# Kernel optimization log

Measured on AMD Instinct MI355X. Metric: run time of the kernel, lower is better.

Reference implementation:

```python
import jax, jax.numpy as jnp
import numpy as np

D_MODEL = 1024
N_HEADS = 16
D_HEAD = D_MODEL // N_HEADS


def setup_inputs() -> dict:
    key = jax.random.key(0)
    k1, k2, k3 = jax.random.split(key, 3)
    x = jax.random.normal(k1, (4, 2048, D_MODEL), dtype=jnp.float32)
    # torch Linear(d, 3d, bias=False): y = x @ W.T with W [3d, d].
    # We store the transposed form W_qkv [d, 3d] so y = x @ W_qkv (same math).
    scale = 1.0 / np.sqrt(D_MODEL)
    W_qkv = jax.random.normal(k2, (D_MODEL, 3 * D_MODEL), dtype=jnp.float32) * scale
    W_o = jax.random.normal(k3, (D_MODEL, D_MODEL), dtype=jnp.float32) * scale
    return {"x": x, "W_qkv": W_qkv, "W_o": W_o}


def reference(x, W_qkv, W_o):
    B, T, C = x.shape
    qkv = x @ W_qkv                              # [B, T, 3C]
    Q, K, V = jnp.split(qkv, 3, axis=-1)
    def to_heads(t):
        return t.reshape(B, T, N_HEADS, D_HEAD).transpose(0, 2, 1, 3)  # [B,H,T,d]
    Q, K, V = to_heads(Q), to_heads(K), to_heads(V)
    scores = jnp.einsum("bhqd,bhkd->bhqk", Q, K) / np.sqrt(D_HEAD)
    attn = jax.nn.softmax(scores, axis=-1)
    # dropout is identity in eval/deterministic mode
    context = jnp.einsum("bhqk,bhkd->bhqd", attn, V)
    context = context.transpose(0, 2, 1, 3).reshape(B, T, C)
    return context @ W_o
```

## Files before the change

kernel.cpp:

```cpp
#include <hip/hip_runtime.h>
#include <hip/hip_bf16.h>

typedef __attribute__((ext_vector_type(8))) short short8;
typedef __attribute__((ext_vector_type(4))) float f32x4;
typedef __attribute__((ext_vector_type(16))) float f32x16;
typedef __attribute__((ext_vector_type(2))) unsigned int uint2v;
typedef __attribute__((ext_vector_type(4))) unsigned int uint4v;

#define SEQ    2048
#define DM     1024
#define NH     16
#define DH     64
#define NBATCH 4
#define MTOK   (NBATCH * SEQ)
#define SEG    ((size_t)NBATCH * NH * SEQ * DH)
#define QSCALE 0.18033688f

static __device__ __forceinline__ unsigned bfbits(float f) {
  unsigned u = __float_as_uint(f);
  return u + 0x7fffu + ((u >> 16) & 1u);
}
static __device__ __forceinline__ unsigned short f2bf(float f) {
  return (unsigned short)(bfbits(f) >> 16);
}
static __device__ __forceinline__ unsigned pack2bf(float lo, float hi) {
  return __builtin_amdgcn_perm(bfbits(hi), bfbits(lo), 0x07060302u);
}
static __device__ __forceinline__ unsigned pack2tr(unsigned ulo, unsigned uhi) {
  return __builtin_amdgcn_perm(uhi, ulo, 0x07060302u);
}

typedef const __attribute__((address_space(1))) unsigned int* gp_t;
typedef __attribute__((address_space(3))) unsigned int* lp_t;
static __device__ __forceinline__ void gload_lds16(const void* g, void* l) {
  __builtin_amdgcn_global_load_lds((gp_t)g, (lp_t)l, 16, 0, 0);
}

__global__ __launch_bounds__(256) void xcast(const float* __restrict__ x,
                                             unsigned short* __restrict__ xb) {
  size_t i = ((size_t)blockIdx.x * 256 + threadIdx.x) * 8;
  f32x4 a = *(const f32x4*)&x[i];
  f32x4 b = *(const f32x4*)&x[i + 4];
  uint4v s;
  s[0] = pack2bf(a[0], a[1]);
  s[1] = pack2bf(a[2], a[3]);
  s[2] = pack2bf(b[0], b[1]);
  s[3] = pack2bf(b[2], b[3]);
  *(uint4v*)&xb[i] = s;
}

__global__ __launch_bounds__(256) void transpose_w(
    const float* __restrict__ W, unsigned short* __restrict__ WT, int K, int N) {
  __shared__ float T[64][65];
  const int tid = threadIdx.x;
  const int n0 = blockIdx.x * 64;
  const int k0 = blockIdx.y * 64;
#pragma unroll
  for (int it = 0; it < 4; it++) {
    int row = it * 16 + (tid >> 4);
    int c4 = (tid & 15) * 4;
    f32x4 v = *(const f32x4*)&W[(size_t)(k0 + row) * N + n0 + c4];
#pragma unroll
    for (int j = 0; j < 4; j++) T[row][c4 + j] = v[j];
  }
  __syncthreads();
#pragma unroll
  for (int it = 0; it < 2; it++) {
    int chunk = tid + it * 256;
    int n = chunk >> 3;
    int c8 = (chunk & 7) * 8;
    uint4v s;
#pragma unroll
    for (int j = 0; j < 4; j++)
      s[j] = pack2bf(T[c8 + 2 * j][n], T[c8 + 2 * j + 1][n]);
    *(uint4v*)&WT[(size_t)(n0 + n) * K + k0 + c8] = s;
  }
}

template <int MODE>
__global__ __launch_bounds__(256) void gemm_kernel(
    const void* __restrict__ Av, const unsigned short* __restrict__ BT,
    unsigned short* __restrict__ out0, unsigned short* __restrict__ out1,
    unsigned short* __restrict__ out2, float* __restrict__ outf,
    int M, int N, int K) {
  __shared__ unsigned short As[128][64];
  __shared__ unsigned short Bs[128][64];

  const int tid = threadIdx.x;
  const int wave = tid >> 6;
  const int lane = tid & 63;
  const int quad = lane >> 4;
  const int lc = lane & 15;
  const int wr = wave >> 1;
  const int wc = wave & 1;
  const int m0 = blockIdx.y * 128;
  const int n0 = blockIdx.x * 128;
  const int xsw = lc & 7;
  const int lr8 = lane >> 3;
  const int sgo = ((lane & 7) ^ (lr8 & 7)) * 8;

  f32x4 acc[4][4];
#pragma unroll
  for (int i = 0; i < 4; i++)
#pragma unroll
    for (int j = 0; j < 4; j++) acc[i][j] = (f32x4){0.f, 0.f, 0.f, 0.f};

  for (int k0 = 0; k0 < K; k0 += 64) {
    if (MODE == 0) {
      const float* A = (const float*)Av;
#pragma unroll
      for (int i = 0; i < 4; i++) {
        int chunk = tid + i * 256;
        int r = chunk >> 3;
        int g = chunk & 7;
        int scol = (g ^ (r & 7)) * 8;
        f32x4 v0 = *(const f32x4*)&A[(size_t)(m0 + r) * K + k0 + scol];
        f32x4 v1 = *(const f32x4*)&A[(size_t)(m0 + r) * K + k0 + scol + 4];
        uint4v s;
        s[0] = pack2bf(v0[0], v0[1]);
        s[1] = pack2bf(v0[2], v0[3]);
        s[2] = pack2bf(v1[0], v1[1]);
        s[3] = pack2bf(v1[2], v1[3]);
        *(uint4v*)&As[r][g * 8] = s;
      }
    } else {
      const unsigned short* A = (const unsigned short*)Av;
#pragma unroll
      for (int it = 0; it < 4; it++) {
        int rbase = wave * 32 + it * 8;
        gload_lds16(&A[(size_t)(m0 + rbase + lr8) * K + k0 + sgo],
                    &As[rbase][0]);
      }
    }
#pragma unroll
    for (int it = 0; it < 4; it++) {
      int rbase = wave * 32 + it * 8;
      gload_lds16(&BT[(size_t)(n0 + rbase + lr8) * K + k0 + sgo],
                  &Bs[rbase][0]);
    }
    __syncthreads();

#pragma unroll
    for (int kc = 0; kc < 2; kc++) {
      short8 aA[4], bB[4];
#pragma unroll
      for (int mt = 0; mt < 4; mt++)
        aA[mt] = *(const short8*)&As[wr * 64 + mt * 16 + lc]
                                    [((kc * 4 + quad) ^ xsw) * 8];
#pragma unroll
      for (int nt = 0; nt < 4; nt++)
        bB[nt] = *(const short8*)&Bs[wc * 64 + nt * 16 + lc]
                                    [((kc * 4 + quad) ^ xsw) * 8];
#pragma unroll
      for (int mt = 0; mt < 4; mt++)
#pragma unroll
        for (int nt = 0; nt < 4; nt++)
          acc[mt][nt] = __builtin_amdgcn_mfma_f32_16x16x32_bf16(
              aA[mt], bB[nt], acc[mt][nt], 0, 0, 0);
    }
    __syncthreads();
  }

  const int c = n0 >> 10;
#pragma unroll
  for (int mt = 0; mt < 4; mt++)
#pragma unroll
    for (int nt = 0; nt < 4; nt++) {
      int rb = m0 + wr * 64 + mt * 16 + quad * 4;
      int col = n0 + wc * 64 + nt * 16 + lc;
      if (MODE == 1) {
#pragma unroll
        for (int r = 0; r < 4; r++)
          outf[(size_t)(rb + r) * N + col] = acc[mt][nt][r];
      } else {
        int rem = col & 1023;
        int h = rem >> 6;
        int dd = rem & 63;
        int b = rb >> 11;
        int tt = rb & 2047;
        if (c == 2) {
          uint2v pk;
          pk[0] = pack2bf(acc[mt][nt][0], acc[mt][nt][1]);
          pk[1] = pack2bf(acc[mt][nt][2], acc[mt][nt][3]);
          *(uint2v*)&out2[(((size_t)(b * NH + h)) * DH + dd) * SEQ + tt] = pk;
        } else {
          unsigned short* dst = (c == 0) ? out0 : out1;
          float sc = (c == 0) ? QSCALE : 1.0f;
#pragma unroll
          for (int r = 0; r < 4; r++)
            dst[(((size_t)(b * NH + h) * SEQ + tt + r) << 6) + dd] =
                f2bf(acc[mt][nt][r] * sc);
        }
      }
    }
}

__global__ __launch_bounds__(256, 4) void attn_kernel(
    const unsigned short* __restrict__ Q, const unsigned short* __restrict__ K,
    const unsigned short* __restrict__ Vt, unsigned short* __restrict__ ctx) {
  __shared__ unsigned short KsL[2][64 * 64];
  __shared__ unsigned short VtL[2][64 * 64];

  const int tid = threadIdx.x;
  const int wave = tid >> 6;
  const int lane = tid & 63;
  const int half = lane >> 5;
  const int l31 = lane & 31;
  const int id = blockIdx.x;
  const int bh = (id & 7) * 8 + (id >> 3) / 16;
  const int qt = (id >> 3) & 15;
  const int q0 = qt * 128 + wave * 32;
  const unsigned kqbase = (unsigned)bh * (SEQ * DH);
  const unsigned vbase = (unsigned)bh * (DH * SEQ);

  short8 bQ[4];
#pragma unroll
  for (int dc = 0; dc < 4; dc++)
    bQ[dc] = *(const short8*)&Q[kqbase + (unsigned)(q0 + l31) * DH + dc * 16 + half * 8];

  f32x16 o[2], o_l;
#pragma unroll
  for (int nb = 0; nb < 2; nb++)
#pragma unroll
    for (int j = 0; j < 16; j++) o[nb][j] = 0.f;
#pragma unroll
  for (int j = 0; j < 16; j++) o_l[j] = 0.f;

  union { unsigned u[4]; short8 s8; } onesu;
#pragma unroll
  for (int j = 0; j < 4; j++) onesu.u[j] = 0x3f803f80u;
  const short8 ones = onesu.s8;

  const int xsw = l31 & 7;
  const int g0 = wave * 128 + lane;
  const int r0 = g0 >> 3;
  const unsigned sgo = ((g0 & 7) ^ (r0 & 7)) * 8;
  const unsigned so0 = (unsigned)r0 * DH + sgo;
  const unsigned sv0 = (unsigned)r0 * SEQ + sgo;
  const int ldo = wave * 1024;

  auto stage = [&](int kt, int b) {
    const unsigned kg = kqbase + (unsigned)kt * (64 * DH);
    const unsigned vg = vbase + (unsigned)kt * 64;
    unsigned short* kd = &KsL[b][ldo];
    unsigned short* vd = &VtL[b][ldo];
    gload_lds16(&K[kg + so0], kd);
    gload_lds16(&K[kg + so0 + 8 * DH], kd + 512);
    gload_lds16(&Vt[vg + sv0], vd);
    gload_lds16(&Vt[vg + sv0 + 8 * SEQ], vd + 512);
  };

  stage(0, 0);
  __syncthreads();

  for (int kt = 0; kt < SEQ / 64; kt++) {
    const int cur = kt & 1;
    if (kt + 1 < SEQ / 64) stage(kt + 1, cur ^ 1);
    const unsigned short* kcur = &KsL[cur][0];
    const unsigned short* vcur = &VtL[cur][0];

#pragma unroll
    for (int kb = 0; kb < 2; kb++) {
      f32x16 s;
#pragma unroll
      for (int j = 0; j < 16; j++) s[j] = 0.f;
      __builtin_amdgcn_s_setprio(1);
#pragma unroll
      for (int dc = 0; dc < 4; dc++) {
        const short8 aK = *(const short8*)&kcur[(unsigned)(kb * 32 + l31) * 64 +
                                                ((dc * 2 + half) ^ xsw) * 8];
        s = __builtin_amdgcn_mfma_f32_32x32x16_bf16(aK, bQ[dc], s, 0, 0, 0);
      }
      __builtin_amdgcn_s_setprio(0);

      unsigned d0[4], d1[4];
#pragma unroll
      for (int gq = 0; gq < 4; gq++) {
        unsigned u0 = __float_as_uint(__builtin_amdgcn_exp2f(s[gq * 4 + 0]));
        unsigned u1 = __float_as_uint(__builtin_amdgcn_exp2f(s[gq * 4 + 1]));
        unsigned u2 = __float_as_uint(__builtin_amdgcn_exp2f(s[gq * 4 + 2]));
        unsigned u3 = __float_as_uint(__builtin_amdgcn_exp2f(s[gq * 4 + 3]));
        d0[gq] = pack2tr(u0, u1);
        d1[gq] = pack2tr(u2, u3);
      }

#pragma unroll
      for (int kcl = 0; kcl < 2; kcl++) {
        unsigned w0 = d0[kcl * 2], w2 = d0[kcl * 2 + 1];
        unsigned w1 = d1[kcl * 2], w3 = d1[kcl * 2 + 1];
        asm("v_permlane32_swap_b32 %0, %1" : "+v"(w0), "+v"(w2));
        asm("v_permlane32_swap_b32 %0, %1" : "+v"(w1), "+v"(w3));
        union { unsigned u[4]; short8 s8; } cv;
        cv.u[0] = w0; cv.u[1] = w1; cv.u[2] = w2; cv.u[3] = w3;
        const int kc = kb * 2 + kcl;
        __builtin_amdgcn_s_setprio(1);
#pragma unroll
        for (int nb = 0; nb < 2; nb++) {
          const short8 bV = *(const short8*)&vcur[(unsigned)(nb * 32 + l31) * 64 +
                                                  ((kc * 2 + half) ^ xsw) * 8];
          o[nb] = __builtin_amdgcn_mfma_f32_32x32x16_bf16(cv.s8, bV, o[nb], 0, 0, 0);
        }
        o_l = __builtin_amdgcn_mfma_f32_32x32x16_bf16(cv.s8, ones, o_l, 0, 0, 0);
        __builtin_amdgcn_s_setprio(0);
      }
    }
    __syncthreads();
  }

  const int b = bh >> 4;
  const int h = bh & 15;
#pragma unroll
  for (int gq = 0; gq < 4; gq++)
#pragma unroll
    for (int j = 0; j < 4; j++) {
      int r = gq * 4 + j;
      int ql = j + gq * 8 + half * 4;
      float inv = __builtin_amdgcn_rcpf(o_l[r]);
      int token = qt * 128 + wave * 32 + ql;
#pragma unroll
      for (int nb = 0; nb < 2; nb++)
        ctx[((size_t)b * SEQ + token) * DM + h * DH + nb * 32 + l31] =
            f2bf(o[nb][r] * inv);
    }
}

extern "C" void kernel_launch(void* const* d_in, const int* in_sizes, int n_in,
                              void* d_out, int out_size, void* d_ws,
                              size_t ws_size, hipStream_t stream) {
  const float* x = (const float*)d_in[0];
  const float* Wqkv = (const float*)d_in[1];
  const float* Wo = (const float*)d_in[2];
  float* out = (float*)d_out;
  unsigned short* ws = (unsigned short*)d_ws;

  unsigned short* Qb = ws;
  unsigned short* Kb = ws + SEG;
  unsigned short* Vt = ws + 2 * SEG;
  unsigned short* Ctx = ws + 3 * SEG;
  unsigned short* WqT = Ctx + (size_t)MTOK * DM;
  unsigned short* WoT = WqT + (size_t)3 * DM * DM;
  unsigned short* Xb = WoT + (size_t)DM * DM;
  const size_t need =
      ((size_t)(Xb - ws) + (size_t)MTOK * DM) * sizeof(unsigned short);

  transpose_w<<<dim3(3 * DM / 64, DM / 64), 256, 0, stream>>>(Wqkv, WqT, DM, 3 * DM);
  transpose_w<<<dim3(DM / 64, DM / 64), 256, 0, stream>>>(Wo, WoT, DM, DM);

  if (ws_size >= need) {
    xcast<<<(MTOK * DM) / (256 * 8), 256, 0, stream>>>(x, Xb);
    gemm_kernel<2><<<dim3(3 * DM / 128, MTOK / 128), 256, 0, stream>>>(
        (const void*)Xb, WqT, Qb, Kb, Vt, nullptr, MTOK, 3 * DM, DM);
  } else {
    gemm_kernel<0><<<dim3(3 * DM / 128, MTOK / 128), 256, 0, stream>>>(
        (const void*)x, WqT, Qb, Kb, Vt, nullptr, MTOK, 3 * DM, DM);
  }
  attn_kernel<<<dim3(SEQ / 128 * NBATCH * NH), 256, 0, stream>>>(Qb, Kb, Vt, Ctx);
  gemm_kernel<1><<<dim3(DM / 128, MTOK / 128), 256, 0, stream>>>(
      (const void*)Ctx, WoT, nullptr, nullptr, nullptr, out, MTOK, DM, DM);
}
```

Measured before the change: 260.2 us.

## Double-buffer GEMM LDS tiles and merge weight/input prep kernels into one launch

The GEMM kernel now keeps two LDS buffers for the A and B tiles. It issues the loads for the next K-tile before running the MFMAs on the current one, so global-to-LDS traffic can overlap with compute. The x cast and the two weight transposes are merged into one prep kernel that picks its work by block index, cutting kernel launches. Doubling shared memory to 64KB per block may lower occupancy, and the overlap depends on how the barrier waits on the asynchronous LDS loads.

```diff
diff --git a/kernel.cpp b/kernel.cpp
--- a/kernel.cpp
+++ b/kernel.cpp
@@ -36,25 +36,40 @@
   __builtin_amdgcn_global_load_lds((gp_t)g, (lp_t)l, 16, 0, 0);
 }
 
-__global__ __launch_bounds__(256) void xcast(const float* __restrict__ x,
-                                             unsigned short* __restrict__ xb) {
-  size_t i = ((size_t)blockIdx.x * 256 + threadIdx.x) * 8;
-  f32x4 a = *(const f32x4*)&x[i];
-  f32x4 b = *(const f32x4*)&x[i + 4];
-  uint4v s;
-  s[0] = pack2bf(a[0], a[1]);
-  s[1] = pack2bf(a[2], a[3]);
-  s[2] = pack2bf(b[0], b[1]);
-  s[3] = pack2bf(b[2], b[3]);
-  *(uint4v*)&xb[i] = s;
-}
-
-__global__ __launch_bounds__(256) void transpose_w(
-    const float* __restrict__ W, unsigned short* __restrict__ WT, int K, int N) {
+template <bool WITH_X>
+__global__ __launch_bounds__(256) void prep_kernel(
+    const float* __restrict__ x, unsigned short* __restrict__ xb,
+    const float* __restrict__ Wqkv, unsigned short* __restrict__ WqT,
+    const float* __restrict__ Wo, unsigned short* __restrict__ WoT) {
   __shared__ float T[64][65];
   const int tid = threadIdx.x;
-  const int n0 = blockIdx.x * 64;
-  const int k0 = blockIdx.y * 64;
+  int bid = blockIdx.x;
+  if (WITH_X) {
+    if (bid < 4096) {
+      size_t i = ((size_t)bid * 256 + tid) * 8;
+      f32x4 a = *(const f32x4*)&x[i];
+      f32x4 b = *(const f32x4*)&x[i + 4];
+      uint4v s;
+      s[0] = pack2bf(a[0], a[1]);
+      s[1] = pack2bf(a[2], a[3]);
+      s[2] = pack2bf(b[0], b[1]);
+      s[3] = pack2bf(b[2], b[3]);
+      *(uint4v*)&xb[i] = s;
+      return;
+    }
+    bid -= 4096;
+  }
+  const float* W;
+  unsigned short* WT;
+  int N, n0, k0;
+  if (bid < 768) {
+    W = Wqkv; WT = WqT; N = 3 * DM;
+    n0 = (bid % 48) * 64; k0 = (bid / 48) * 64;
+  } else {
+    bid -= 768;
+    W = Wo; WT = WoT; N = DM;
+    n0 = (bid % 16) * 64; k0 = (bid / 16) * 64;
+  }
 #pragma unroll
   for (int it = 0; it < 4; it++) {
     int row = it * 16 + (tid >> 4);
@@ -73,7 +88,7 @@
 #pragma unroll
     for (int j = 0; j < 4; j++)
       s[j] = pack2bf(T[c8 + 2 * j][n], T[c8 + 2 * j + 1][n]);
-    *(uint4v*)&WT[(size_t)(n0 + n) * K + k0 + c8] = s;
+    *(uint4v*)&WT[(size_t)(n0 + n) * DM + k0 + c8] = s;
   }
 }
 
@@ -83,8 +98,8 @@
     unsigned short* __restrict__ out0, unsigned short* __restrict__ out1,
     unsigned short* __restrict__ out2, float* __restrict__ outf,
     int M, int N, int K) {
-  __shared__ unsigned short As[128][64];
-  __shared__ unsigned short Bs[128][64];
+  __shared__ unsigned short As[2][128][64];
+  __shared__ unsigned short Bs[2][128][64];
 
   const int tid = threadIdx.x;
   const int wave = tid >> 6;
@@ -105,7 +120,9 @@
 #pragma unroll
     for (int j = 0; j < 4; j++) acc[i][j] = (f32x4){0.f, 0.f, 0.f, 0.f};
 
-  for (int k0 = 0; k0 < K; k0 += 64) {
+  const int NKT = K >> 6;
+
+  auto stage = [&](int k0, int buf) {
     if (MODE == 0) {
       const float* A = (const float*)Av;
 #pragma unroll
@@ -121,7 +138,7 @@
         s[1] = pack2bf(v0[2], v0[3]);
         s[2] = pack2bf(v1[0], v1[1]);
         s[3] = pack2bf(v1[2], v1[3]);
-        *(uint4v*)&As[r][g * 8] = s;
+        *(uint4v*)&As[buf][r][g * 8] = s;
       }
     } else {
       const unsigned short* A = (const unsigned short*)Av;
@@ -129,27 +146,34 @@
       for (int it = 0; it < 4; it++) {
         int rbase = wave * 32 + it * 8;
         gload_lds16(&A[(size_t)(m0 + rbase + lr8) * K + k0 + sgo],
-                    &As[rbase][0]);
+                    &As[buf][rbase][0]);
       }
     }
 #pragma unroll
     for (int it = 0; it < 4; it++) {
       int rbase = wave * 32 + it * 8;
       gload_lds16(&BT[(size_t)(n0 + rbase + lr8) * K + k0 + sgo],
-                  &Bs[rbase][0]);
-    }
-    __syncthreads();
+                  &Bs[buf][rbase][0]);
+    }
+  };
+
+  stage(0, 0);
+  __syncthreads();
+
+  for (int kt = 0; kt < NKT; kt++) {
+    const int cur = kt & 1;
+    if (kt + 1 < NKT) stage((kt + 1) * 64, cur ^ 1);
 
 #pragma unroll
     for (int kc = 0; kc < 2; kc++) {
       short8 aA[4], bB[4];
 #pragma unroll
       for (int mt = 0; mt < 4; mt++)
-        aA[mt] = *(const short8*)&As[wr * 64 + mt * 16 + lc]
+        aA[mt] = *(const short8*)&As[cur][wr * 64 + mt * 16 + lc]
                                     [((kc * 4 + quad) ^ xsw) * 8];
 #pragma unroll
       for (int nt = 0; nt < 4; nt++)
-        bB[nt] = *(const short8*)&Bs[wc * 64 + nt * 16 + lc]
+        bB[nt] = *(const short8*)&Bs[cur][wc * 64 + nt * 16 + lc]
                                     [((kc * 4 + quad) ^ xsw) * 8];
 #pragma unroll
       for (int mt = 0; mt < 4; mt++)
@@ -343,14 +367,14 @@
   const size_t need =
       ((size_t)(Xb - ws) + (size_t)MTOK * DM) * sizeof(unsigned short);
 
-  transpose_w<<<dim3(3 * DM / 64, DM / 64), 256, 0, stream>>>(Wqkv, WqT, DM, 3 * DM);
-  transpose_w<<<dim3(DM / 64, DM / 64), 256, 0, stream>>>(Wo, WoT, DM, DM);
-
   if (ws_size >= need) {
-    xcast<<<(MTOK * DM) / (256 * 8), 256, 0, stream>>>(x, Xb);
+    prep_kernel<true><<<dim3(4096 + 768 + 256), 256, 0, stream>>>(
+        x, Xb, Wqkv, WqT, Wo, WoT);
     gemm_kernel<2><<<dim3(3 * DM / 128, MTOK / 128), 256, 0, stream>>>(
         (const void*)Xb, WqT, Qb, Kb, Vt, nullptr, MTOK, 3 * DM, DM);
   } else {
+    prep_kernel<false><<<dim3(768 + 256), 256, 0, stream>>>(
+        x, nullptr, Wqkv, WqT, Wo, WoT);
     gemm_kernel<0><<<dim3(3 * DM / 128, MTOK / 128), 256, 0, stream>>>(
         (const void*)x, WqT, Qb, Kb, Vt, nullptr, MTOK, 3 * DM, DM);
   }
```

New measurement: 266.3 us. 2.3% more time.
